# Optimization experiments

Hardware: AMD Instinct MI355X
Metric: run time of the kernel (lower is better)

## Reference

```python
import jax, jax.numpy as jnp
import numpy as np

B, N, F = 16, 2048, 128      # graphs, padded nodes, input feature dim
HID, FC, C = 32, 512, 10     # GCN width, dense hidden, num_classes


def setup_inputs() -> dict:
    key = jax.random.key(0)
    ks = jax.random.split(key, 9)
    filtre = jax.random.uniform(ks[0], (B, N, N), dtype=jnp.float32)       # normalized adjacency filter
    X = jax.random.normal(ks[1], (B, N, F), dtype=jnp.float32)             # node features
    node_indicator = jax.random.randint(ks[2], (B, N), 0, 2, dtype=jnp.int32)
    # learned parameters (Glorot-ish scaling)
    W1 = jax.random.normal(ks[3], (F, HID), dtype=jnp.float32) / np.sqrt(F)
    b1 = jnp.zeros((HID,), dtype=jnp.float32)
    Ws = jax.random.normal(ks[4], (HID, 1), dtype=jnp.float32) / np.sqrt(HID)  # DiffPool assignment, max_clusters=1
    Wd = jax.random.normal(ks[5], (HID, FC), dtype=jnp.float32) / np.sqrt(HID)
    bd = jnp.zeros((FC,), dtype=jnp.float32)
    Wc = jax.random.normal(ks[6], (FC, C), dtype=jnp.float32) / np.sqrt(FC)
    bc = jnp.zeros((C,), dtype=jnp.float32)
    return {"filtre": filtre, "X": X, "node_indicator": node_indicator,
            "W1": W1, "b1": b1, "Ws": Ws, "Wd": Wd, "bd": bd, "Wc": Wc, "bc": bc}


def reference(filtre, X, node_indicator, W1, b1, Ws, Wd, bd, Wc, bc):
    # GCN layer: H = relu(A @ X @ W1 + b1)   [B, N, HID]  (dropout inactive at inference)
    H = jax.nn.relu(jnp.einsum('bnm,bmf->bnf', filtre, X) @ W1 + b1)
    # DiffPool assignment to 1 cluster: S = softmax(A @ H @ Ws) over cluster axis  [B, N, 1]
    S = jax.nn.softmax(jnp.einsum('bnm,bmh->bnh', filtre, H) @ Ws, axis=-1)
    # pooled features X' = S^T H  [B, 1, HID]  (pooled adjacency S^T A S is unused downstream)
    Xp = jnp.einsum('bnk,bnh->bkh', S, H)
    # dense head
    h = jax.nn.relu(Xp @ Wd + bd)                # [B, 1, FC]
    return jax.nn.softmax(h @ Wc + bc, axis=-1)  # [B, 1, C]
```

## Files before the change

kernel.cpp:

```cpp
#include <hip/hip_runtime.h>
#include <hip/hip_bf16.h>


#define B_   16
#define N_   2048
#define F_   128
#define HID_ 32
#define FC_  512
#define C_   10

typedef __bf16 bf16x8 __attribute__((ext_vector_type(8)));
typedef float  f32x4  __attribute__((ext_vector_type(4)));
typedef float  floatx4 __attribute__((ext_vector_type(4)));

__global__ __launch_bounds__(256) void k1_xw(
    const float* __restrict__ X, const float* __restrict__ W1,
    __bf16* __restrict__ XWT, float* __restrict__ Xp)
{
    const int tid = threadIdx.x;
    if (blockIdx.x == 0) {
        for (int i = tid; i < B_ * HID_; i += 256) Xp[i] = 0.f;
    }
    const int b   = blockIdx.x >> 4;
    const int seg = blockIdx.x & 15;
    const int w    = tid >> 6;
    const int lane = tid & 63;
    const int r = lane & 15, q = lane >> 4;

    bf16x8 wf[2][4];
    #pragma unroll
    for (int t = 0; t < 2; ++t) {
        const int h = r + 16 * t;
        #pragma unroll
        for (int ks = 0; ks < 4; ++ks) {
            bf16x8 v;
            #pragma unroll
            for (int j = 0; j < 8; ++j) {
                const int f = ks * 32 + q * 8 + j;
                v[j] = (__bf16)W1[f * HID_ + h];
            }
            wf[t][ks] = v;
        }
    }

    #pragma unroll
    for (int i = 0; i < 2; ++i) {
        const int m0 = seg * 128 + w * 16 + i * 64;
        const int m  = m0 + r;
        const floatx4* xrow = (const floatx4*)(X + ((size_t)(b * N_ + m)) * F_);
        f32x4 acc0 = {0.f, 0.f, 0.f, 0.f};
        f32x4 acc1 = {0.f, 0.f, 0.f, 0.f};
        #pragma unroll
        for (int ks = 0; ks < 4; ++ks) {
            floatx4 x0 = xrow[ks * 8 + q * 2];
            floatx4 x1 = xrow[ks * 8 + q * 2 + 1];
            bf16x8 bf;
            bf[0] = (__bf16)x0[0]; bf[1] = (__bf16)x0[1];
            bf[2] = (__bf16)x0[2]; bf[3] = (__bf16)x0[3];
            bf[4] = (__bf16)x1[0]; bf[5] = (__bf16)x1[1];
            bf[6] = (__bf16)x1[2]; bf[7] = (__bf16)x1[3];
            acc0 = __builtin_amdgcn_mfma_f32_16x16x32_bf16(wf[0][ks], bf, acc0, 0, 0, 0);
            acc1 = __builtin_amdgcn_mfma_f32_16x16x32_bf16(wf[1][ks], bf, acc1, 0, 0, 0);
        }
        #pragma unroll
        for (int reg = 0; reg < 4; ++reg) {
            const int h0 = q * 4 + reg;
            XWT[((size_t)(b * HID_ + h0)) * N_ + m]      = (__bf16)acc0[reg];
            XWT[((size_t)(b * HID_ + h0 + 16)) * N_ + m] = (__bf16)acc1[reg];
        }
    }
}

__global__ __launch_bounds__(128) void k2_axw(
    const float* __restrict__ A, const __bf16* __restrict__ XWT,
    const float* __restrict__ b1, float* __restrict__ Xp)
{
    const int tid = threadIdx.x;
    const int b       = blockIdx.x >> 6;
    const int rowBase = (blockIdx.x & 63) * 32;
    const int w    = tid >> 6;
    const int lane = tid & 63;
    const int r = lane & 15, q = lane >> 4;
    const int row = rowBase + w * 16 + r;

    const floatx4* arow = (const floatx4*)(A + ((size_t)b * N_ + row) * (size_t)N_);
    const bf16x8* bp0 = (const bf16x8*)(XWT + ((size_t)(b * HID_ + r)) * N_);
    const bf16x8* bp1 = (const bf16x8*)(XWT + ((size_t)(b * HID_ + r + 16)) * N_);

    f32x4 acc0 = {0.f, 0.f, 0.f, 0.f};
    f32x4 acc1 = {0.f, 0.f, 0.f, 0.f};

    #pragma unroll 4
    for (int ks = 0; ks < N_ / 32; ++ks) {
        floatx4 a0 = arow[ks * 8 + q * 2];
        floatx4 a1 = arow[ks * 8 + q * 2 + 1];
        bf16x8 af;
        af[0] = (__bf16)a0[0]; af[1] = (__bf16)a0[1];
        af[2] = (__bf16)a0[2]; af[3] = (__bf16)a0[3];
        af[4] = (__bf16)a1[0]; af[5] = (__bf16)a1[1];
        af[6] = (__bf16)a1[2]; af[7] = (__bf16)a1[3];
        bf16x8 bf0 = bp0[ks * 4 + q];
        bf16x8 bf1 = bp1[ks * 4 + q];
        acc0 = __builtin_amdgcn_mfma_f32_16x16x32_bf16(af, bf0, acc0, 0, 0, 0);
        acc1 = __builtin_amdgcn_mfma_f32_16x16x32_bf16(af, bf1, acc1, 0, 0, 0);
    }

    const float bias0 = b1[r], bias1 = b1[r + 16];
    float s0 = 0.f, s1 = 0.f;
    #pragma unroll
    for (int reg = 0; reg < 4; ++reg) {
        s0 += fmaxf(acc0[reg] + bias0, 0.f);
        s1 += fmaxf(acc1[reg] + bias1, 0.f);
    }
    s0 += __shfl_xor(s0, 16); s0 += __shfl_xor(s0, 32);
    s1 += __shfl_xor(s1, 16); s1 += __shfl_xor(s1, 32);

    __shared__ float sdata[2][HID_];
    if (lane < 16) { sdata[w][r] = s0; sdata[w][r + 16] = s1; }
    __syncthreads();
    if (tid < HID_) {
        atomicAdd(&Xp[b * HID_ + tid], sdata[0][tid] + sdata[1][tid]);
    }
}

__global__ __launch_bounds__(256) void k3_head(
    const float* __restrict__ Xp, const float* __restrict__ Wd,
    const float* __restrict__ bd, const float* __restrict__ Wc,
    const float* __restrict__ bc, float* __restrict__ out)
{
    __shared__ float xp[HID_];
    __shared__ float hbuf[FC_];
    __shared__ float logits[C_];
    const int b = blockIdx.x;
    const int t = threadIdx.x;

    if (t < HID_) xp[t] = Xp[b * HID_ + t];
    __syncthreads();

    for (int f = t; f < FC_; f += 256) {
        float acc = bd[f];
        #pragma unroll
        for (int j = 0; j < HID_; ++j) acc += xp[j] * Wd[j * FC_ + f];
        hbuf[f] = fmaxf(acc, 0.f);
    }
    __syncthreads();

    if (t < 16 * C_) {
        const int c = t >> 4, l = t & 15;
        float acc = 0.f;
        for (int f = l; f < FC_; f += 16) acc += hbuf[f] * Wc[f * C_ + c];
        acc += __shfl_xor(acc, 8, 16);
        acc += __shfl_xor(acc, 4, 16);
        acc += __shfl_xor(acc, 2, 16);
        acc += __shfl_xor(acc, 1, 16);
        if (l == 0) logits[c] = acc + bc[c];
    }
    __syncthreads();

    if (t == 0) {
        float mx = logits[0];
        #pragma unroll
        for (int c = 1; c < C_; ++c) mx = fmaxf(mx, logits[c]);
        float e[C_]; float sum = 0.f;
        #pragma unroll
        for (int c = 0; c < C_; ++c) { e[c] = expf(logits[c] - mx); sum += e[c]; }
        const float inv = 1.f / sum;
        #pragma unroll
        for (int c = 0; c < C_; ++c) out[b * C_ + c] = e[c] * inv;
    }
}

extern "C" void kernel_launch(void* const* d_in, const int* in_sizes, int n_in,
                              void* d_out, int out_size, void* d_ws, size_t ws_size,
                              hipStream_t stream) {
    const float* filtre = (const float*)d_in[0];
    const float* X      = (const float*)d_in[1];
    const float* W1     = (const float*)d_in[3];
    const float* b1     = (const float*)d_in[4];
    const float* Wd     = (const float*)d_in[6];
    const float* bd     = (const float*)d_in[7];
    const float* Wc     = (const float*)d_in[8];
    const float* bc     = (const float*)d_in[9];
    float* out = (float*)d_out;

    __bf16* XWT = (__bf16*)d_ws;
    float*  Xp  = (float*)((char*)d_ws + (size_t)B_ * HID_ * N_ * sizeof(__bf16));

    k1_xw <<<256,  256, 0, stream>>>(X, W1, XWT, Xp);
    k2_axw<<<1024, 128, 0, stream>>>(filtre, XWT, b1, Xp);
    k3_head<<<B_,  256, 0, stream>>>(Xp, Wd, bd, Wc, bc, out);
}
```

Baseline: 423.7 us.

## Stream adjacency tiles into LDS via async DMA with multi-stage prefetch

The A@XW kernel now uses global_load_lds to copy fp32 adjacency tiles straight into a 4-slot LDS ring buffer, prefetching two chunks ahead. Each wave waits on vmcnt only for its own tile before reading it from LDS. The LDS layout is XOR-swizzled to avoid bank conflicts. Blocks grow to 256 threads covering 64 rows. The aim is to keep more memory requests in flight on the dominant 268 MB stream of A and hide load latency behind the MFMA work. The cost is hand-coded waitcnt values, which are fragile if the compiler inserts or reorders other vector-memory ops, and more LDS per block, which may lower occupancy.

```diff
diff --git a/kernel.cpp b/kernel.cpp
--- a/kernel.cpp
+++ b/kernel.cpp
@@ -12,6 +12,13 @@
 typedef __bf16 bf16x8 __attribute__((ext_vector_type(8)));
 typedef float  f32x4  __attribute__((ext_vector_type(4)));
 typedef float  floatx4 __attribute__((ext_vector_type(4)));
+
+typedef const __attribute__((address_space(1))) void* as1_cvp;
+typedef __attribute__((address_space(3))) void*       as3_vp;
+
+__device__ static __forceinline__ void dma16(void* lds_uniform, const void* g) {
+    __builtin_amdgcn_global_load_lds((as1_cvp)g, (as3_vp)lds_uniform, 16, 0, 0);
+}
 
 __global__ __launch_bounds__(256) void k1_xw(
     const float* __restrict__ X, const float* __restrict__ W1,
@@ -71,38 +78,72 @@
     }
 }
 
-__global__ __launch_bounds__(128) void k2_axw(
+__global__ __launch_bounds__(256, 2) void k2_axw(
     const float* __restrict__ A, const __bf16* __restrict__ XWT,
     const float* __restrict__ b1, float* __restrict__ Xp)
 {
-    const int tid = threadIdx.x;
-    const int b       = blockIdx.x >> 6;
-    const int rowBase = (blockIdx.x & 63) * 32;
+    __shared__ __align__(16) float abuf[4][4][16 * 64];
+    __shared__ float sdata[4][HID_];
+
+    const int tid  = threadIdx.x;
     const int w    = tid >> 6;
     const int lane = tid & 63;
     const int r = lane & 15, q = lane >> 4;
-    const int row = rowBase + w * 16 + r;
-
-    const floatx4* arow = (const floatx4*)(A + ((size_t)b * N_ + row) * (size_t)N_);
+    const int rs = r & 7;
+
+    const int b       = blockIdx.x >> 5;
+    const int rowBase = (blockIdx.x & 31) * 64;
+    const int row0    = rowBase + w * 16;
+
+    const int rl = lane >> 4;
+    const int ch = lane & 15;
+
     const bf16x8* bp0 = (const bf16x8*)(XWT + ((size_t)(b * HID_ + r)) * N_);
     const bf16x8* bp1 = (const bf16x8*)(XWT + ((size_t)(b * HID_ + r + 16)) * N_);
 
     f32x4 acc0 = {0.f, 0.f, 0.f, 0.f};
     f32x4 acc1 = {0.f, 0.f, 0.f, 0.f};
 
-    #pragma unroll 4
-    for (int ks = 0; ks < N_ / 32; ++ks) {
-        floatx4 a0 = arow[ks * 8 + q * 2];
-        floatx4 a1 = arow[ks * 8 + q * 2 + 1];
-        bf16x8 af;
-        af[0] = (__bf16)a0[0]; af[1] = (__bf16)a0[1];
-        af[2] = (__bf16)a0[2]; af[3] = (__bf16)a0[3];
-        af[4] = (__bf16)a1[0]; af[5] = (__bf16)a1[1];
-        af[6] = (__bf16)a1[2]; af[7] = (__bf16)a1[3];
-        bf16x8 bf0 = bp0[ks * 4 + q];
-        bf16x8 bf1 = bp1[ks * 4 + q];
-        acc0 = __builtin_amdgcn_mfma_f32_16x16x32_bf16(af, bf0, acc0, 0, 0, 0);
-        acc1 = __builtin_amdgcn_mfma_f32_16x16x32_bf16(af, bf1, acc1, 0, 0, 0);
+    auto stage = [&](int c) {
+        const int t = c & 3;
+        #pragma unroll
+        for (int j = 0; j < 4; ++j) {
+            const int rlocal = j * 4 + rl;
+            const int gchunk = ch ^ (rlocal & 7);
+            const size_t gelem = ((size_t)(b * N_ + row0 + rlocal)) * N_
+                               + (size_t)c * 64 + (size_t)(gchunk * 4);
+            dma16((void*)&abuf[t][w][j * 256], (const void*)(A + gelem));
+        }
+    };
+
+    auto compute = [&](int c) {
+        const int t = c & 3;
+        const float* aw = &abuf[t][w][0];
+        #pragma unroll
+        for (int kl = 0; kl < 2; ++kl) {
+            const int s0 = (kl * 8 + q * 2) ^ rs;
+            const floatx4 u0 = *(const floatx4*)(aw + r * 64 + s0 * 4);
+            const floatx4 u1 = *(const floatx4*)(aw + r * 64 + (s0 ^ 1) * 4);
+            bf16x8 af;
+            af[0] = (__bf16)u0[0]; af[1] = (__bf16)u0[1];
+            af[2] = (__bf16)u0[2]; af[3] = (__bf16)u0[3];
+            af[4] = (__bf16)u1[0]; af[5] = (__bf16)u1[1];
+            af[6] = (__bf16)u1[2]; af[7] = (__bf16)u1[3];
+            const int ksg = c * 2 + kl;
+            bf16x8 bf0 = bp0[ksg * 4 + q];
+            bf16x8 bf1 = bp1[ksg * 4 + q];
+            acc0 = __builtin_amdgcn_mfma_f32_16x16x32_bf16(af, bf0, acc0, 0, 0, 0);
+            acc1 = __builtin_amdgcn_mfma_f32_16x16x32_bf16(af, bf1, acc1, 0, 0, 0);
+        }
+    };
+
+    stage(0);
+    stage(1);
+    for (int c = 0; c < 32; ++c) {
+        if (c + 2 < 32) stage(c + 2);
+        if (c + 1 < 32) __builtin_amdgcn_s_waitcnt(0x0F74);
+        else            __builtin_amdgcn_s_waitcnt(0x0F70);
+        compute(c);
     }
 
     const float bias0 = b1[r], bias1 = b1[r + 16];
@@ -115,11 +156,11 @@
     s0 += __shfl_xor(s0, 16); s0 += __shfl_xor(s0, 32);
     s1 += __shfl_xor(s1, 16); s1 += __shfl_xor(s1, 32);
 
-    __shared__ float sdata[2][HID_];
     if (lane < 16) { sdata[w][r] = s0; sdata[w][r + 16] = s1; }
     __syncthreads();
     if (tid < HID_) {
-        atomicAdd(&Xp[b * HID_ + tid], sdata[0][tid] + sdata[1][tid]);
+        atomicAdd(&Xp[b * HID_ + tid],
+                  sdata[0][tid] + sdata[1][tid] + sdata[2][tid] + sdata[3][tid]);
     }
 }
 
@@ -186,7 +227,7 @@
     __bf16* XWT = (__bf16*)d_ws;
     float*  Xp  = (float*)((char*)d_ws + (size_t)B_ * HID_ * N_ * sizeof(__bf16));
 
-    k1_xw <<<256,  256, 0, stream>>>(X, W1, XWT, Xp);
-    k2_axw<<<1024, 128, 0, stream>>>(filtre, XWT, b1, Xp);
+    k1_xw <<<256, 256, 0, stream>>>(X, W1, XWT, Xp);
+    k2_axw<<<512, 256, 0, stream>>>(filtre, XWT, b1, Xp);
     k3_head<<<B_,  256, 0, stream>>>(Xp, Wd, bd, Wc, bc, out);
 }
```

Result: no change. 416.4 us (-1.7%).
